# Kernel optimization log

Measured on AMD Instinct MI355X. Metric: run time of the kernel, lower is better.

Reference implementation:

```python
import jax, jax.numpy as jnp
import numpy as np

N_NODES = 10000
IN_C = 32
OUT_C = 32
EDGE_F = 16
N_EDGES = 320000


def setup_inputs() -> dict:
    key = jax.random.key(0)
    ks = jax.random.split(key, 6)
    x = jax.random.normal(ks[0], (N_NODES, IN_C), dtype=jnp.float32)
    edge_index = jax.random.randint(ks[1], (2, N_EDGES), 0, N_NODES, dtype=jnp.int64)
    edge_attr = jax.random.normal(ks[2], (N_EDGES, EDGE_F), dtype=jnp.float32)
    # edge MLP (ff_unit): Linear(edge_features, in*out) + ReLU
    W_edge = jax.random.normal(ks[3], (EDGE_F, IN_C * OUT_C), dtype=jnp.float32) * (1.0 / np.sqrt(EDGE_F))
    b_edge = jnp.zeros((IN_C * OUT_C,), dtype=jnp.float32)
    # NNConv root (self-loop) weight and bias
    root = jax.random.normal(ks[4], (IN_C, OUT_C), dtype=jnp.float32) * (1.0 / np.sqrt(IN_C))
    bias = jnp.zeros((OUT_C,), dtype=jnp.float32)
    return {"x": x, "edge_index": edge_index, "edge_attr": edge_attr,
            "W_edge": W_edge, "b_edge": b_edge, "root": root, "bias": bias}


def reference(x, edge_index, edge_attr, W_edge, b_edge, root, bias):
    E = edge_attr.shape[0]
    N = x.shape[0]
    # edge MLP -> per-edge weight matrix [E, in, out]
    w = jax.nn.relu(edge_attr @ W_edge + b_edge).reshape(E, IN_C, OUT_C)
    src = edge_index[0]  # source node j
    dst = edge_index[1]  # target node i
    # message: x_j @ Theta(e_ij)  -> [E, out]
    msg = jnp.einsum('ei,eio->eo', x[src], w)
    # mean aggregation over incoming edges per target node
    summed = jax.ops.segment_sum(msg, dst, num_segments=N)
    cnt = jax.ops.segment_sum(jnp.ones((E,), x.dtype), dst, num_segments=N)
    aggr = summed / jnp.maximum(cnt, 1.0)[:, None]
    # update: aggr + x @ root + bias (PyG NNConv)
    return aggr + x @ root + bias
```

## Files before the change

### kernel.cpp

```cpp
#include <hip/hip_runtime.h>
#include <hip/hip_bf16.h>

#define NN 10000
#define INC 32
#define OUTC 32
#define EF 16
#define NE 320000
#define CAP 96

typedef __attribute__((ext_vector_type(8)))  __bf16 bf16x8;
typedef __attribute__((ext_vector_type(16))) float  f32x16;
typedef __attribute__((ext_vector_type(4)))  float  f32x4;

__global__ void scatter_bucket_kernel(const int* __restrict__ eidx,
                                      int* __restrict__ cnt, int2* __restrict__ bucket) {
    for (int e = blockIdx.x * 256 + threadIdx.x; e < NE; e += gridDim.x * 256) {
        int d = eidx[NE + e];
        int s = eidx[e];
        int p = atomicAdd(&cnt[d], 1);
        if (p < CAP) bucket[d * CAP + p] = make_int2(e, s);
    }
}

__global__ __launch_bounds__(256, 3) void edge_node_kernel(
    const float* __restrict__ x, const float* __restrict__ ea,
    const float* __restrict__ W, const float* __restrict__ be,
    const float* __restrict__ root, const float* __restrict__ bias,
    const int* __restrict__ cnt, const int2* __restrict__ bucket,
    float* __restrict__ out)
{
    __shared__ __attribute__((aligned(16))) __bf16 WT[32][2][32][8];
    __shared__ __attribute__((aligned(16))) float  BPF[32][2][16];
    __shared__ __attribute__((aligned(16))) float  root_s[32][32];
    __shared__ float bias_s[32];
    __shared__ float msum[4][32];

    const int tid = threadIdx.x;

    #pragma unroll
    for (int k = 0; k < 8; ++k) {
        int idx = tid + k * 256;
        int cb = idx >> 6, rem = idx & 63, hi2 = rem >> 5, c = rem & 31;
        int cg = cb * 32 + c;
        #pragma unroll
        for (int j = 0; j < 8; ++j)
            WT[cb][hi2][c][j] = (__bf16)W[(8 * hi2 + j) * 1024 + cg];
    }
    #pragma unroll
    for (int k = 0; k < 4; ++k) {
        int idx = tid + k * 256;
        int cb = idx >> 5, rem = idx & 31, hi2 = rem >> 4, r = rem & 15;
        int row = (r & 3) + 8 * (r >> 2) + 4 * hi2;
        BPF[cb][hi2][r] = be[cb * 32 + row];
        root_s[idx >> 5][idx & 31] = root[idx];
    }
    if (tid < 32) bias_s[tid] = bias[tid];
    __syncthreads();

    const int lane = tid & 63;
    const int hi   = lane >> 5;
    const int l31  = lane & 31;
    const int w    = tid >> 6;
    const int n    = blockIdx.x * 4 + w;

    const int deg = cnt[n];
    const int2* bk = bucket + (size_t)n * CAP;

    float msgr[16];
    #pragma unroll
    for (int r = 0; r < 16; ++r) msgr[r] = 0.0f;

    for (int c0 = 0; c0 < deg; c0 += 32) {
        const int idx  = c0 + l31;
        const bool act = idx < deg;
        const int2 es  = bk[act ? idx : deg - 1];
        const int e    = es.x;
        const int src  = es.y;

        const f32x4* eap = (const f32x4*)(ea + e * 16 + hi * 8);
        f32x4 f0 = eap[0];
        f32x4 f1 = eap[1];
        bf16x8 bfrag;
        bfrag[0] = (__bf16)f0.x; bfrag[1] = (__bf16)f0.y;
        bfrag[2] = (__bf16)f0.z; bfrag[3] = (__bf16)f0.w;
        bfrag[4] = (__bf16)f1.x; bfrag[5] = (__bf16)f1.y;
        bfrag[6] = (__bf16)f1.z; bfrag[7] = (__bf16)f1.w;

        const float4* xp = (const float4*)(x + src * 32);

        int base = 0;
        asm volatile("" : "+v"(base));

        #pragma unroll
        for (int cbq = 0; cbq < 8; ++cbq) {
            float4 xq = xp[cbq];
            if (!act) { xq.x = 0.0f; xq.y = 0.0f; xq.z = 0.0f; xq.w = 0.0f; }
            #pragma unroll
            for (int c4 = 0; c4 < 4; ++c4) {
                const int g = cbq * 4 + c4;
                bf16x8 af = *(const bf16x8*)(&WT[base + g][hi][l31][0]);
                f32x16 ci = *(const f32x16*)(&BPF[base + g][hi][0]);
                f32x16 acc = __builtin_amdgcn_mfma_f32_32x32x16_bf16(af, bfrag, ci, 0, 0, 0);
                const float xv = (c4 == 0) ? xq.x : (c4 == 1) ? xq.y : (c4 == 2) ? xq.z : xq.w;
                #pragma unroll
                for (int r = 0; r < 16; ++r)
                    msgr[r] += fmaxf(acc[r], 0.0f) * xv;
                if (c4 & 1) __builtin_amdgcn_sched_barrier(0);
            }
        }
    }

    #pragma unroll
    for (int m = 1; m <= 16; m <<= 1) {
        #pragma unroll
        for (int r = 0; r < 16; ++r)
            msgr[r] += __shfl_xor(msgr[r], m, 64);
    }

    const float rdeg = (deg > 0) ? (1.0f / (float)deg) : 0.0f;
    if (l31 == 0) {
        #pragma unroll
        for (int r = 0; r < 16; ++r) {
            const int o = (r & 3) + 8 * (r >> 2) + 4 * hi;
            msum[w][o] = msgr[r] * rdeg;
        }
    }
    __syncthreads();

    const float xv = x[(size_t)n * 32 + l31];
    if (hi == 0) {
        float m = msum[w][l31] + bias_s[l31];
        #pragma unroll
        for (int i = 0; i < 32; ++i)
            m += __shfl(xv, i, 64) * root_s[i][l31];
        out[(size_t)n * 32 + l31] = m;
    }
}

extern "C" void kernel_launch(void* const* d_in, const int* in_sizes, int n_in,
                              void* d_out, int out_size, void* d_ws, size_t ws_size,
                              hipStream_t stream) {
    const float* x    = (const float*)d_in[0];
    const int*   eidx = (const int*)d_in[1];
    const float* ea   = (const float*)d_in[2];
    const float* W    = (const float*)d_in[3];
    const float* be   = (const float*)d_in[4];
    const float* root = (const float*)d_in[5];
    const float* bias = (const float*)d_in[6];
    float* out = (float*)d_out;

    int*  cnt    = (int*)d_ws;
    int2* bucket = (int2*)((char*)d_ws + ((NN * 4 + 15) & ~15));

    hipMemsetAsync(cnt, 0, NN * sizeof(int), stream);
    scatter_bucket_kernel<<<640, 256, 0, stream>>>(eidx, cnt, bucket);
    edge_node_kernel<<<NN / 4, 256, 0, stream>>>(x, ea, W, be, root, bias,
                                                 cnt, bucket, out);
}
```

Measured before the change: 100.2 us.

## Switch edge MLP to 16x16x32 MFMA with bias folded into K

Replaces the 32x32x16 MFMA (K=16 edge features, bias loaded as the accumulator input) with 16x16x32 MFMAs. The bias is folded into the padded K dimension through a constant-one feature lane, and each wave handles two 16-edge groups per instruction pair. This shrinks the per-lane accumulator and message register footprint (16 floats down to 8), which allows raising launch bounds to 4 blocks per SM, and x loads are software-prefetched one float4 ahead. In exchange, half of the K dimension is zero padding, so MFMA work per edge roughly doubles, and the bias is now rounded to bf16.

Measured after the change: 142.9 us. 42.6% more time.

```diff
diff --git a/kernel.cpp b/kernel.cpp
--- a/kernel.cpp
+++ b/kernel.cpp
@@ -2,14 +2,10 @@
 #include <hip/hip_bf16.h>
 
 #define NN 10000
-#define INC 32
-#define OUTC 32
-#define EF 16
 #define NE 320000
 #define CAP 96
 
 typedef __attribute__((ext_vector_type(8)))  __bf16 bf16x8;
-typedef __attribute__((ext_vector_type(16))) float  f32x16;
 typedef __attribute__((ext_vector_type(4)))  float  f32x4;
 
 __global__ void scatter_bucket_kernel(const int* __restrict__ eidx,
@@ -22,111 +18,129 @@
     }
 }
 
-__global__ __launch_bounds__(256, 3) void edge_node_kernel(
+__global__ __launch_bounds__(256, 4) void edge_node_kernel(
     const float* __restrict__ x, const float* __restrict__ ea,
     const float* __restrict__ W, const float* __restrict__ be,
     const float* __restrict__ root, const float* __restrict__ bias,
     const int* __restrict__ cnt, const int2* __restrict__ bucket,
     float* __restrict__ out)
 {
-    __shared__ __attribute__((aligned(16))) __bf16 WT[32][2][32][8];
-    __shared__ __attribute__((aligned(16))) float  BPF[32][2][16];
+    __shared__ __attribute__((aligned(16))) __bf16 WT2[64][2][16][8];
+    __shared__ __attribute__((aligned(16))) __bf16 BRL[1024];
     __shared__ __attribute__((aligned(16))) float  root_s[32][32];
     __shared__ float bias_s[32];
     __shared__ float msum[4][32];
 
     const int tid = threadIdx.x;
 
-    #pragma unroll
-    for (int k = 0; k < 8; ++k) {
-        int idx = tid + k * 256;
-        int cb = idx >> 6, rem = idx & 63, hi2 = rem >> 5, c = rem & 31;
-        int cg = cb * 32 + c;
-        #pragma unroll
-        for (int j = 0; j < 8; ++j)
-            WT[cb][hi2][c][j] = (__bf16)W[(8 * hi2 + j) * 1024 + cg];
+    for (int u = tid; u < 16384; u += 256) {
+        int j = u & 7, cl = (u >> 3) & 15, kg = (u >> 7) & 1, ct = u >> 8;
+        WT2[ct][kg][cl][j] = (__bf16)W[(kg * 8 + j) * 1024 + ct * 16 + cl];
     }
-    #pragma unroll
-    for (int k = 0; k < 4; ++k) {
-        int idx = tid + k * 256;
-        int cb = idx >> 5, rem = idx & 31, hi2 = rem >> 4, r = rem & 15;
-        int row = (r & 3) + 8 * (r >> 2) + 4 * hi2;
-        BPF[cb][hi2][r] = be[cb * 32 + row];
-        root_s[idx >> 5][idx & 31] = root[idx];
+    for (int u = tid; u < 1024; u += 256) {
+        BRL[u] = (__bf16)be[u];
+        root_s[u >> 5][u & 31] = root[u];
     }
     if (tid < 32) bias_s[tid] = bias[tid];
     __syncthreads();
 
     const int lane = tid & 63;
-    const int hi   = lane >> 5;
-    const int l31  = lane & 31;
+    const int kgrp = lane >> 4;
+    const int c16  = lane & 15;
     const int w    = tid >> 6;
     const int n    = blockIdx.x * 4 + w;
 
     const int deg = cnt[n];
     const int2* bk = bucket + (size_t)n * CAP;
 
-    float msgr[16];
-    #pragma unroll
-    for (int r = 0; r < 16; ++r) msgr[r] = 0.0f;
+    float ms0[4] = {0.f, 0.f, 0.f, 0.f};
+    float ms1[4] = {0.f, 0.f, 0.f, 0.f};
 
     for (int c0 = 0; c0 < deg; c0 += 32) {
-        const int idx  = c0 + l31;
-        const bool act = idx < deg;
-        const int2 es  = bk[act ? idx : deg - 1];
-        const int e    = es.x;
-        const int src  = es.y;
+        const int i0 = c0 + c16, i1 = i0 + 16;
+        const bool a0 = i0 < deg, a1 = i1 < deg;
+        const int2 es0 = bk[a0 ? i0 : deg - 1];
+        const int2 es1 = bk[a1 ? i1 : deg - 1];
 
-        const f32x4* eap = (const f32x4*)(ea + e * 16 + hi * 8);
-        f32x4 f0 = eap[0];
-        f32x4 f1 = eap[1];
-        bf16x8 bfrag;
-        bfrag[0] = (__bf16)f0.x; bfrag[1] = (__bf16)f0.y;
-        bfrag[2] = (__bf16)f0.z; bfrag[3] = (__bf16)f0.w;
-        bfrag[4] = (__bf16)f1.x; bfrag[5] = (__bf16)f1.y;
-        bfrag[6] = (__bf16)f1.z; bfrag[7] = (__bf16)f1.w;
+        bf16x8 bf0 = {}, bf1 = {};
+        if (kgrp < 2) {
+            const f32x4* p0 = (const f32x4*)(ea + (size_t)es0.x * 16 + kgrp * 8);
+            const f32x4* p1 = (const f32x4*)(ea + (size_t)es1.x * 16 + kgrp * 8);
+            f32x4 u0 = p0[0], u1 = p0[1], v0 = p1[0], v1 = p1[1];
+            bf0[0]=(__bf16)u0.x; bf0[1]=(__bf16)u0.y; bf0[2]=(__bf16)u0.z; bf0[3]=(__bf16)u0.w;
+            bf0[4]=(__bf16)u1.x; bf0[5]=(__bf16)u1.y; bf0[6]=(__bf16)u1.z; bf0[7]=(__bf16)u1.w;
+            bf1[0]=(__bf16)v0.x; bf1[1]=(__bf16)v0.y; bf1[2]=(__bf16)v0.z; bf1[3]=(__bf16)v0.w;
+            bf1[4]=(__bf16)v1.x; bf1[5]=(__bf16)v1.y; bf1[6]=(__bf16)v1.z; bf1[7]=(__bf16)v1.w;
+        } else if (kgrp == 2) {
+            bf0[0] = (__bf16)1.0f;
+            bf1[0] = (__bf16)1.0f;
+        }
+        if (!a0) bf0 = (bf16x8){};
+        if (!a1) bf1 = (bf16x8){};
 
-        const float4* xp = (const float4*)(x + src * 32);
+        const f32x4* xp0 = (const f32x4*)(x + (size_t)es0.y * 32);
+        const f32x4* xp1 = (const f32x4*)(x + (size_t)es1.y * 32);
 
-        int base = 0;
-        asm volatile("" : "+v"(base));
-
-        #pragma unroll
-        for (int cbq = 0; cbq < 8; ++cbq) {
-            float4 xq = xp[cbq];
-            if (!act) { xq.x = 0.0f; xq.y = 0.0f; xq.z = 0.0f; xq.w = 0.0f; }
+        int ib0 = 0;
+        asm volatile("" : "+v"(ib0));
+        f32x4 xq0 = xp0[0], xq1 = xp1[0];
+        #pragma unroll 1
+        for (int ib = ib0; ib < 8; ++ib) {
+            f32x4 nx0 = xq0, nx1 = xq1;
+            if (ib < 7) { nx0 = xp0[ib + 1]; nx1 = xp1[ib + 1]; }
             #pragma unroll
-            for (int c4 = 0; c4 < 4; ++c4) {
-                const int g = cbq * 4 + c4;
-                bf16x8 af = *(const bf16x8*)(&WT[base + g][hi][l31][0]);
-                f32x16 ci = *(const f32x16*)(&BPF[base + g][hi][0]);
-                f32x16 acc = __builtin_amdgcn_mfma_f32_32x32x16_bf16(af, bfrag, ci, 0, 0, 0);
-                const float xv = (c4 == 0) ? xq.x : (c4 == 1) ? xq.y : (c4 == 2) ? xq.z : xq.w;
-                #pragma unroll
-                for (int r = 0; r < 16; ++r)
-                    msgr[r] += fmaxf(acc[r], 0.0f) * xv;
-                if (c4 & 1) __builtin_amdgcn_sched_barrier(0);
+            for (int cc = 0; cc < 8; ++cc) {
+                const int ct = ib * 8 + cc;
+                bf16x8 af;
+                if (kgrp < 2) {
+                    af = *(const bf16x8*)(&WT2[ct][kgrp][c16][0]);
+                } else {
+                    af = (bf16x8){};
+                    if (kgrp == 2) af[0] = BRL[ct * 16 + c16];
+                }
+                const f32x4 z = {0.0f, 0.0f, 0.0f, 0.0f};
+                f32x4 A0 = __builtin_amdgcn_mfma_f32_16x16x32_bf16(af, bf0, z, 0, 0, 0);
+                f32x4 A1 = __builtin_amdgcn_mfma_f32_16x16x32_bf16(af, bf1, z, 0, 0, 0);
+                const float xv0 = (cc >> 1) == 0 ? xq0.x : (cc >> 1) == 1 ? xq0.y
+                                : (cc >> 1) == 2 ? xq0.z : xq0.w;
+                const float xv1 = (cc >> 1) == 0 ? xq1.x : (cc >> 1) == 1 ? xq1.y
+                                : (cc >> 1) == 2 ? xq1.z : xq1.w;
+                if (cc & 1) {
+                    #pragma unroll
+                    for (int r = 0; r < 4; ++r)
+                        ms1[r] += fmaxf(A0[r], 0.0f) * xv0 + fmaxf(A1[r], 0.0f) * xv1;
+                } else {
+                    #pragma unroll
+                    for (int r = 0; r < 4; ++r)
+                        ms0[r] += fmaxf(A0[r], 0.0f) * xv0 + fmaxf(A1[r], 0.0f) * xv1;
+                }
+                if ((cc & 3) == 3) __builtin_amdgcn_sched_barrier(0);
             }
+            xq0 = nx0; xq1 = nx1;
         }
     }
 
     #pragma unroll
-    for (int m = 1; m <= 16; m <<= 1) {
+    for (int mm = 1; mm <= 8; mm <<= 1) {
         #pragma unroll
-        for (int r = 0; r < 16; ++r)
-            msgr[r] += __shfl_xor(msgr[r], m, 64);
+        for (int r = 0; r < 4; ++r) {
+            ms0[r] += __shfl_xor(ms0[r], mm, 64);
+            ms1[r] += __shfl_xor(ms1[r], mm, 64);
+        }
     }
 
     const float rdeg = (deg > 0) ? (1.0f / (float)deg) : 0.0f;
-    if (l31 == 0) {
+    if (c16 == 0) {
         #pragma unroll
-        for (int r = 0; r < 16; ++r) {
-            const int o = (r & 3) + 8 * (r >> 2) + 4 * hi;
-            msum[w][o] = msgr[r] * rdeg;
+        for (int r = 0; r < 4; ++r) {
+            msum[w][kgrp * 4 + r]      = ms0[r] * rdeg;
+            msum[w][16 + kgrp * 4 + r] = ms1[r] * rdeg;
         }
     }
     __syncthreads();
 
+    const int hi  = lane >> 5;
+    const int l31 = lane & 31;
     const float xv = x[(size_t)n * 32 + l31];
     if (hi == 0) {
         float m = msum[w][l31] + bias_s[l31];
```

## Precompute bf16 edge weights once in scatter kernel and read from global

Applied to the files above, without the earlier changes.

Adds an extra block to the scatter kernel that converts W_edge to a bf16 layout matching the MFMA A-fragment, written into workspace. The edge kernel no longer rebuilds the 32KB bf16 weight table in shared memory in each of its 2500 blocks; it reads the fragments straight from global/L2 instead. This cuts per-block prologue work and LDS use, which also permits raising launch bounds to 4 blocks per CU. The trade-off is that every MFMA now takes its A operand from a global load rather than LDS, which may add latency in the inner loop.

After: 105.2 us. 1.05x slower.

```diff
diff --git a/kernel.cpp b/kernel.cpp
--- a/kernel.cpp
+++ b/kernel.cpp
@@ -2,9 +2,6 @@
 #include <hip/hip_bf16.h>
 
 #define NN 10000
-#define INC 32
-#define OUTC 32
-#define EF 16
 #define NE 320000
 #define CAP 96
 
@@ -13,8 +10,16 @@
 typedef __attribute__((ext_vector_type(4)))  float  f32x4;
 
 __global__ void scatter_bucket_kernel(const int* __restrict__ eidx,
-                                      int* __restrict__ cnt, int2* __restrict__ bucket) {
-    for (int e = blockIdx.x * 256 + threadIdx.x; e < NE; e += gridDim.x * 256) {
+                                      int* __restrict__ cnt, int2* __restrict__ bucket,
+                                      const float* __restrict__ W, __bf16* __restrict__ wbf) {
+    if (blockIdx.x == 640) {
+        for (int u = threadIdx.x; u < 16384; u += 256) {
+            int j = u & 7, c = (u >> 3) & 31, hi = (u >> 8) & 1, g = u >> 9;
+            wbf[u] = (__bf16)W[(hi * 8 + j) * 1024 + g * 32 + c];
+        }
+        return;
+    }
+    for (int e = blockIdx.x * 256 + threadIdx.x; e < NE; e += 640 * 256) {
         int d = eidx[NE + e];
         int s = eidx[e];
         int p = atomicAdd(&cnt[d], 1);
@@ -22,30 +27,20 @@
     }
 }
 
-__global__ __launch_bounds__(256, 3) void edge_node_kernel(
+__global__ __launch_bounds__(256, 4) void edge_node_kernel(
     const float* __restrict__ x, const float* __restrict__ ea,
-    const float* __restrict__ W, const float* __restrict__ be,
+    const __bf16* __restrict__ wbf, const float* __restrict__ be,
     const float* __restrict__ root, const float* __restrict__ bias,
     const int* __restrict__ cnt, const int2* __restrict__ bucket,
     float* __restrict__ out)
 {
-    __shared__ __attribute__((aligned(16))) __bf16 WT[32][2][32][8];
-    __shared__ __attribute__((aligned(16))) float  BPF[32][2][16];
-    __shared__ __attribute__((aligned(16))) float  root_s[32][32];
+    __shared__ __attribute__((aligned(16))) float BPF[32][2][16];
+    __shared__ __attribute__((aligned(16))) float root_s[32][32];
     __shared__ float bias_s[32];
     __shared__ float msum[4][32];
 
     const int tid = threadIdx.x;
 
-    #pragma unroll
-    for (int k = 0; k < 8; ++k) {
-        int idx = tid + k * 256;
-        int cb = idx >> 6, rem = idx & 63, hi2 = rem >> 5, c = rem & 31;
-        int cg = cb * 32 + c;
-        #pragma unroll
-        for (int j = 0; j < 8; ++j)
-            WT[cb][hi2][c][j] = (__bf16)W[(8 * hi2 + j) * 1024 + cg];
-    }
     #pragma unroll
     for (int k = 0; k < 4; ++k) {
         int idx = tid + k * 256;
@@ -65,6 +60,7 @@
 
     const int deg = cnt[n];
     const int2* bk = bucket + (size_t)n * CAP;
+    const __bf16* wb = wbf + hi * 256 + l31 * 8;
 
     float msgr[16];
     #pragma unroll
@@ -77,7 +73,7 @@
         const int e    = es.x;
         const int src  = es.y;
 
-        const f32x4* eap = (const f32x4*)(ea + e * 16 + hi * 8);
+        const f32x4* eap = (const f32x4*)(ea + (size_t)e * 16 + hi * 8);
         f32x4 f0 = eap[0];
         f32x4 f1 = eap[1];
         bf16x8 bfrag;
@@ -86,7 +82,7 @@
         bfrag[4] = (__bf16)f1.x; bfrag[5] = (__bf16)f1.y;
         bfrag[6] = (__bf16)f1.z; bfrag[7] = (__bf16)f1.w;
 
-        const float4* xp = (const float4*)(x + src * 32);
+        const float4* xp = (const float4*)(x + (size_t)src * 32);
 
         int base = 0;
         asm volatile("" : "+v"(base));
@@ -98,7 +94,7 @@
             #pragma unroll
             for (int c4 = 0; c4 < 4; ++c4) {
                 const int g = cbq * 4 + c4;
-                bf16x8 af = *(const bf16x8*)(&WT[base + g][hi][l31][0]);
+                bf16x8 af = *(const bf16x8*)(wb + (size_t)(base + g) * 512);
                 f32x16 ci = *(const f32x16*)(&BPF[base + g][hi][0]);
                 f32x16 acc = __builtin_amdgcn_mfma_f32_32x32x16_bf16(af, bfrag, ci, 0, 0, 0);
                 const float xv = (c4 == 0) ? xq.x : (c4 == 1) ? xq.y : (c4 == 2) ? xq.z : xq.w;
@@ -149,11 +145,12 @@
     const float* bias = (const float*)d_in[6];
     float* out = (float*)d_out;
 
-    int*  cnt    = (int*)d_ws;
-    int2* bucket = (int2*)((char*)d_ws + ((NN * 4 + 15) & ~15));
+    int*    cnt    = (int*)d_ws;
+    int2*   bucket = (int2*)((char*)d_ws + 40000);
+    __bf16* wbf    = (__bf16*)((char*)d_ws + 40000 + (size_t)NN * CAP * 8);
 
     hipMemsetAsync(cnt, 0, NN * sizeof(int), stream);
-    scatter_bucket_kernel<<<640, 256, 0, stream>>>(eidx, cnt, bucket);
-    edge_node_kernel<<<NN / 4, 256, 0, stream>>>(x, ea, W, be, root, bias,
+    scatter_bucket_kernel<<<641, 256, 0, stream>>>(eidx, cnt, bucket, W, wbf);
+    edge_node_kernel<<<NN / 4, 256, 0, stream>>>(x, ea, wbf, be, root, bias,
                                                  cnt, bucket, out);
 }
```

## Software-pipeline LDS fragment loads, prefetch x rows, coalesce W staging

Applied to the files above, without the earlier changes.

Restructures the inner MFMA loop to double-buffer the LDS weight and bias fragments, loading the next group's fragments while the current MFMA and ReLU-FMA epilogue run. All eight x-row float4 loads are hoisted ahead of the loop, and the launch bound is relaxed from 3 to 2 waves per SIMD to make room for the extra registers. The W-to-LDS staging now uses coalesced float4 reads. The cost is higher register pressure and lower occupancy, which may hurt latency hiding for the gathers.

After: 135.1 us. 34.8% more time.

```diff
diff --git a/kernel.cpp b/kernel.cpp
--- a/kernel.cpp
+++ b/kernel.cpp
@@ -2,9 +2,6 @@
 #include <hip/hip_bf16.h>
 
 #define NN 10000
-#define INC 32
-#define OUTC 32
-#define EF 16
 #define NE 320000
 #define CAP 96
 
@@ -22,7 +19,7 @@
     }
 }
 
-__global__ __launch_bounds__(256, 3) void edge_node_kernel(
+__global__ __launch_bounds__(256, 2) void edge_node_kernel(
     const float* __restrict__ x, const float* __restrict__ ea,
     const float* __restrict__ W, const float* __restrict__ be,
     const float* __restrict__ root, const float* __restrict__ bias,
@@ -37,14 +34,19 @@
 
     const int tid = threadIdx.x;
 
-    #pragma unroll
-    for (int k = 0; k < 8; ++k) {
-        int idx = tid + k * 256;
-        int cb = idx >> 6, rem = idx & 63, hi2 = rem >> 5, c = rem & 31;
-        int cg = cb * 32 + c;
+    {
+        const f32x4* Wv = (const f32x4*)W;
         #pragma unroll
-        for (int j = 0; j < 8; ++j)
-            WT[cb][hi2][c][j] = (__bf16)W[(8 * hi2 + j) * 1024 + cg];
+        for (int t = 0; t < 16; ++t) {
+            int u4 = tid + t * 256;
+            f32x4 w4 = Wv[u4];
+            int k = u4 >> 8, c0 = (u4 & 255) * 4;
+            #pragma unroll
+            for (int q = 0; q < 4; ++q) {
+                int cg = c0 + q;
+                WT[cg >> 5][k >> 3][cg & 31][k & 7] = (__bf16)w4[q];
+            }
+        }
     }
     #pragma unroll
     for (int k = 0; k < 4; ++k) {
@@ -74,39 +76,45 @@
         const int idx  = c0 + l31;
         const bool act = idx < deg;
         const int2 es  = bk[act ? idx : deg - 1];
-        const int e    = es.x;
-        const int src  = es.y;
 
-        const f32x4* eap = (const f32x4*)(ea + e * 16 + hi * 8);
+        const f32x4* eap = (const f32x4*)(ea + (size_t)es.x * 16 + hi * 8);
         f32x4 f0 = eap[0];
         f32x4 f1 = eap[1];
+        const f32x4* xp = (const f32x4*)(x + (size_t)es.y * 32);
+        f32x4 xq[8];
+        #pragma unroll
+        for (int q = 0; q < 8; ++q) xq[q] = xp[q];
+
         bf16x8 bfrag;
-        bfrag[0] = (__bf16)f0.x; bfrag[1] = (__bf16)f0.y;
-        bfrag[2] = (__bf16)f0.z; bfrag[3] = (__bf16)f0.w;
-        bfrag[4] = (__bf16)f1.x; bfrag[5] = (__bf16)f1.y;
-        bfrag[6] = (__bf16)f1.z; bfrag[7] = (__bf16)f1.w;
+        bfrag[0]=(__bf16)f0.x; bfrag[1]=(__bf16)f0.y; bfrag[2]=(__bf16)f0.z; bfrag[3]=(__bf16)f0.w;
+        bfrag[4]=(__bf16)f1.x; bfrag[5]=(__bf16)f1.y; bfrag[6]=(__bf16)f1.z; bfrag[7]=(__bf16)f1.w;
 
-        const float4* xp = (const float4*)(x + src * 32);
+        if (!act) {
+            #pragma unroll
+            for (int q = 0; q < 8; ++q) { xq[q].x=0.f; xq[q].y=0.f; xq[q].z=0.f; xq[q].w=0.f; }
+        }
 
         int base = 0;
         asm volatile("" : "+v"(base));
 
+        bf16x8 afA = *(const bf16x8*)(&WT[base][hi][l31][0]);
+        f32x16 ciA = *(const f32x16*)(&BPF[base][hi][0]);
         #pragma unroll
-        for (int cbq = 0; cbq < 8; ++cbq) {
-            float4 xq = xp[cbq];
-            if (!act) { xq.x = 0.0f; xq.y = 0.0f; xq.z = 0.0f; xq.w = 0.0f; }
+        for (int g = 0; g < 32; ++g) {
+            bf16x8 afB = afA;
+            f32x16 ciB = ciA;
+            if (g < 31) {
+                afB = *(const bf16x8*)(&WT[base + g + 1][hi][l31][0]);
+                ciB = *(const f32x16*)(&BPF[base + g + 1][hi][0]);
+            }
+            f32x16 acc = __builtin_amdgcn_mfma_f32_32x32x16_bf16(afA, bfrag, ciA, 0, 0, 0);
+            const float xv = xq[g >> 2][g & 3];
             #pragma unroll
-            for (int c4 = 0; c4 < 4; ++c4) {
-                const int g = cbq * 4 + c4;
-                bf16x8 af = *(const bf16x8*)(&WT[base + g][hi][l31][0]);
-                f32x16 ci = *(const f32x16*)(&BPF[base + g][hi][0]);
-                f32x16 acc = __builtin_amdgcn_mfma_f32_32x32x16_bf16(af, bfrag, ci, 0, 0, 0);
-                const float xv = (c4 == 0) ? xq.x : (c4 == 1) ? xq.y : (c4 == 2) ? xq.z : xq.w;
-                #pragma unroll
-                for (int r = 0; r < 16; ++r)
-                    msgr[r] += fmaxf(acc[r], 0.0f) * xv;
-                if (c4 & 1) __builtin_amdgcn_sched_barrier(0);
-            }
+            for (int r = 0; r < 16; ++r)
+                msgr[r] += fmaxf(acc[r], 0.0f) * xv;
+            __builtin_amdgcn_sched_barrier(0);
+            afA = afB;
+            ciA = ciB;
         }
     }
 
```
